# Kernel optimization log

Measured on AMD Instinct MI355X. Metric: run time of the kernel, lower is better.

The kernel has to match this reference:

```python
import jax, jax.numpy as jnp
import numpy as np

D0, D1 = 512, 512          # PSF / sensor dims (DIMS0, DIMS1)
P0, P1 = D0 // 2, D1 // 2  # pad sizes
ITERS = 20
MU1, MU2, MU3 = 1e-6, 1e-5, 1e-5
TAU = 1e-4 * 1000.0        # 0.1, as in module


def _ct(x):  # zero-pad crop-adjoint: sensor -> full size
    return jnp.pad(x, [(0, 0)] * (x.ndim - 2) + [(P0, P0), (P1, P1)])


def _c(x):  # crop full -> sensor size
    return x[..., P0:P0 + D0, P1:P1 + D1]


def _fft2(x):
    return jnp.fft.fft2(x, axes=(-2, -1))


def _ifft2(x):
    return jnp.fft.ifft2(x, axes=(-2, -1))


def _ifftshift(x):
    return jnp.fft.ifftshift(x, axes=(-2, -1))


def _fftshift(x):
    return jnp.fft.fftshift(x, axes=(-2, -1))


def _H(x, Hf):  # forward blur operator
    return jnp.real(_fftshift(_ifft2(Hf * _fft2(_ifftshift(x)))))


def _Hadj(x, Hf):  # adjoint blur operator
    return jnp.real(_fftshift(_ifft2(jnp.conj(Hf) * _fft2(_ifftshift(x)))))


def _psi(x):  # finite differences stacked on last axis -> (..., 2)
    return jnp.stack([jnp.roll(x, 1, axis=-2) - x,
                      jnp.roll(x, 1, axis=-1) - x], axis=-1)


def _psit(u):  # adjoint of _psi
    d0, d1 = u[..., 0], u[..., 1]
    return (jnp.roll(d0, -1, axis=-2) - d0) + (jnp.roll(d1, -1, axis=-1) - d1)


def _soft(v, thresh):
    return jnp.sign(v) * jnp.maximum(jnp.abs(v) - thresh, 0.0)


def _make_ltl():  # FFT of laplacian kernel (Psi^T Psi in Fourier domain)
    lapl = np.zeros((2 * D0, 2 * D1), np.float32)
    lapl[0, 0] = 4.0
    lapl[0, 1] = -1.0
    lapl[1, 0] = -1.0
    lapl[0, -1] = -1.0
    lapl[-1, 0] = -1.0
    return jnp.fft.fft2(jnp.asarray(lapl))


def setup_inputs() -> dict:
    key = jax.random.key(0)
    k1, k2 = jax.random.split(key)
    y = jax.random.uniform(k1, (8, 1, D0, D1), dtype=jnp.float32)
    h = jax.random.uniform(k2, (D0, D1), dtype=jnp.float32)
    return {"y": y, "h": h}


def reference(y, h):
    Hf = _fft2(_ifftshift(_ct(h[None])))            # (1, 2D0, 2D1) complex
    LtL = _make_ltl()                               # (2D0, 2D1) complex
    Vdiv = 1.0 / (_ct(jnp.ones((1, 1, D0, D1), y.dtype)) + MU1)
    Rdiv = 1.0 / (MU1 * jnp.abs(jnp.conj(Hf) * Hf) + MU2 * jnp.abs(LtL) + MU3)
    CTy = _ct(y)                                    # (B,1,2D0,2D1)

    B = y.shape[0]
    full = (B, 1, 2 * D0, 2 * D1)
    X = jnp.zeros(full, y.dtype)
    U = jnp.zeros(full + (2,), y.dtype)
    V = jnp.zeros(full, y.dtype)
    W = jnp.zeros(full, y.dtype)
    a1 = jnp.zeros(full, y.dtype)
    a2 = jnp.zeros(full + (2,), y.dtype)
    a3 = jnp.zeros(full, y.dtype)

    def step(carry, _):
        X, U, V, W, a1, a2, a3 = carry
        U = _soft(_psi(X) + a2 / MU2, TAU / MU2)
        V = Vdiv * (a1 + MU1 * _H(X, Hf) + CTy)
        W = jnp.maximum(a3 / MU3 + X, 0.0)
        r = (MU3 * W - a3) + _psit(MU2 * U - a2) + _Hadj(MU1 * V - a1, Hf)
        X = jnp.real(_fftshift(_ifft2(Rdiv * _fft2(_ifftshift(r)))))
        a1 = a1 + MU1 * (_H(X, Hf) - V)
        a2 = a2 + MU2 * (_psi(X) - U)
        a3 = a3 + MU3 * (X - W)
        return (X, U, V, W, a1, a2, a3), None

    (X, _, _, _, _, _, _), _ = jax.lax.scan(step, (X, U, V, W, a1, a2, a3), None, length=ITERS)
    return _c(X)
```

## Files before the change

### kernel.cpp

```cpp
#include <hip/hip_runtime.h>
#include <math.h>

#define N 1024
#define NN (1024*1024)
#define BATCH 8

static constexpr float MU1 = 1e-6f, MU2 = 1e-5f, MU3 = 1e-5f;

__device__ __forceinline__ float2 cmulf(float2 a, float2 b){
  return make_float2(a.x*b.x - a.y*b.y, a.x*b.y + a.y*b.x);
}
__device__ __forceinline__ float softf(float v, float T){
  float a = fmaxf(fabsf(v) - T, 0.f);
  return copysignf(a, v);
}
__device__ __forceinline__ int rev4_10(int p){
  return ((p&3)<<8) | (((p>>2)&3)<<6) | (((p>>4)&3)<<4) | (((p>>6)&3)<<2) | ((p>>8)&3);
}
__device__ __forceinline__ int foldc(int k){
  if (k == 0) return 0;
  if (k == 512) return 1;
  return (k < 512) ? 2*k : 2*(1024-k)+1;
}
__device__ __forceinline__ int unfoldc(int c){
  if (c < 2) return c ? 512 : 0;
  return (c & 1) ? 1024 - ((c-1)>>1) : (c>>1);
}

template<int DIR>
__device__ __forceinline__ void fft1024(float2* bufA, float2* bufB,
                                        const float2* Ws, int tid){
  float2* cur = bufA; float2* oth = bufB;
  int s = 1;
  for (int st = 0; st < 10; ++st){
    int m = 512 >> st;
    #pragma unroll
    for (int bb = 0; bb < 2; ++bb){
      int b = tid + bb*256;
      int p = b >> st;
      int q = b & (s-1);
      float2 a = cur[b];
      float2 c = cur[b + 512];
      float2 w = Ws[b & ~(s-1)];
      if (DIR > 0) w.y = -w.y;
      float2 d = make_float2(a.x - c.x, a.y - c.y);
      oth[q + s*(2*p)]   = make_float2(a.x + c.x, a.y + c.y);
      oth[q + s*(2*p+1)] = cmulf(d, w);
    }
    __syncthreads();
    float2* t = cur; cur = oth; oth = t;
    s <<= 1;
  }
}

__global__ void k_twiddle(float2* W){
  int j = blockIdx.x*blockDim.x + threadIdx.x;
  if (j < 768){
    double a = -2.0 * M_PI * (double)j / 1024.0;
    W[j] = make_float2((float)cos(a), (float)sin(a));
  }
}

__global__ void k_build_h(const float* __restrict__ h, float2* __restrict__ Z){
  int idx = blockIdx.x*256 + threadIdx.x;
  int i = idx >> 10, j = idx & 1023;
  float v = 0.f;
  if (i >= 256 && i < 768 && j >= 256 && j < 768)
    v = h[(i-256)*512 + (j-256)];
  Z[idx] = make_float2(v, 0.f);
}

__global__ void k_filters2(const float2* __restrict__ ZT, float2* __restrict__ HfC,
                           float* __restrict__ RdC){
  int id = blockIdx.x*256 + threadIdx.x;
  int p = id >> 10, cp = id & 1023;
  int ki = rev4_10(p);
  int kj = unfoldc(cp);
  float2 v = ZT[((size_t)kj << 10) | (size_t)ki];
  float sgn = ((ki + kj) & 1) ? -1.f : 1.f;
  HfC[id] = make_float2(sgn*v.x, sgn*v.y);
  double mag2 = (double)v.x*(double)v.x + (double)v.y*(double)v.y;
  double ltl = 4.0 - 2.0*cos(2.0*M_PI*(double)ki/1024.0)
                   - 2.0*cos(2.0*M_PI*(double)kj/1024.0);
  double rd = 1.0 / ((double)MU1*mag2 + (double)MU2*ltl + (double)MU3);
  RdC[id] = (float)(rd / ((double)N * (double)N));
}

__global__ void k_init(float* __restrict__ X, float* __restrict__ G0,
                       float* __restrict__ G1, float* __restrict__ K,
                       float* __restrict__ M, const float* __restrict__ y){
  int idx = blockIdx.x*256 + threadIdx.x;
  int e = idx >> 20, r = (idx >> 10) & 1023, c = idx & 1023;
  X[idx] = 0.f; G0[idx] = 0.f; G1[idx] = 0.f; K[idx] = 0.f;
  float m = 0.f;
  if (r >= 256 && r < 768 && c >= 256 && c < 768)
    m = y[(size_t)e*262144 + (size_t)(r-256)*512 + (c-256)] * (MU1/(1.f + MU1));
  M[idx] = m;
}

__global__ void k_ka(const float* __restrict__ X, float* __restrict__ G0,
                     float* __restrict__ G1){
  int idx = blockIdx.x*256 + threadIdx.x;
  int e = idx >> 20, r = (idx >> 10) & 1023, c = idx & 1023;
  size_t eb = (size_t)e * NN;
  float x   = X[idx];
  float xmr = X[eb + (size_t)((r-1)&1023)*N + c];
  float xmc = X[eb + (size_t)r*N + ((c-1)&1023)];
  float psi0 = xmr - x, psi1 = xmc - x;
  float g0 = G0[idx], g1 = G1[idx];
  const float T = 1e4f;
  float u0 = softf(2.f*psi0 - g0*(1.f/MU2), T);
  float u1 = softf(2.f*psi1 - g1*(1.f/MU2), T);
  G0[idx] = MU2*(u0 - psi0) + g0;
  G1[idx] = MU2*(u1 - psi1) + g1;
}

__global__ __launch_bounds__(256) void k_p1(const float* __restrict__ G0,
                                            const float* __restrict__ G1,
                                            const float* __restrict__ K,
                                            const float* __restrict__ M,
                                            float2* __restrict__ Z,
                                            const float2* __restrict__ Wg, int e0){
  __shared__ float2 bufA[N], bufB[N], Ws[512];
  int tid = threadIdx.x;
  int i = blockIdx.x, c = blockIdx.y, e = e0 + c;
  size_t rb  = (size_t)e*NN + (size_t)i*N;
  size_t rb1 = (size_t)e*NN + (size_t)((i+1)&1023)*N;
  size_t zb  = (size_t)c*NN + (size_t)i*N;
  for (int k = tid; k < 512; k += 256) Ws[k] = Wg[k];
  for (int j = tid; j < N; j += 256){
    int jp = (j+1) & 1023;
    float s = K[rb+j] + (G0[rb1+j] - G0[rb+j]) + (G1[rb+jp] - G1[rb+j]);
    bufA[j] = make_float2(s, M[rb+j]);
  }
  __syncthreads();
  fft1024<-1>(bufA, bufB, Ws, tid);
  for (int j = tid; j < N; j += 256) bufB[foldc(j)] = bufA[j];
  __syncthreads();
  for (int j = tid; j < N; j += 256) Z[zb+j] = bufB[j];
}

template<int DIR>
__global__ __launch_bounds__(256) void k_fft_row(float2* Z, const float2* __restrict__ Wg){
  __shared__ float2 bufA[N], bufB[N], Ws[512];
  int tid = threadIdx.x;
  size_t base = ((size_t)blockIdx.y * N + blockIdx.x) * N;
  for (int k = tid; k < 512; k += 256) Ws[k] = Wg[k];
  for (int k = tid; k < N; k += 256) bufA[k] = Z[base + k];
  __syncthreads();
  fft1024<DIR>(bufA, bufB, Ws, tid);
  for (int k = tid; k < N; k += 256) Z[base + k] = bufA[k];
}

__global__ void k_transpose_ip(float2* Z){
  __shared__ float2 ta[32][33], tb[32][33];
  int t = blockIdx.x, ti = 0;
  while (t >= 32 - ti){ t -= 32 - ti; ti++; }
  int tj = ti + t;
  size_t base = (size_t)blockIdx.y * NN;
  int ra = ti*32, ca = tj*32;
  for (int k = threadIdx.y; k < 32; k += 8){
    ta[k][threadIdx.x] = Z[base + (size_t)(ra+k)*N + ca + threadIdx.x];
    if (ti != tj)
      tb[k][threadIdx.x] = Z[base + (size_t)(ca+k)*N + ra + threadIdx.x];
  }
  __syncthreads();
  for (int k = threadIdx.y; k < 32; k += 8){
    Z[base + (size_t)(ra+k)*N + ca + threadIdx.x] = (ti!=tj) ? tb[threadIdx.x][k]
                                                             : ta[threadIdx.x][k];
    if (ti != tj)
      Z[base + (size_t)(ca+k)*N + ra + threadIdx.x] = ta[threadIdx.x][k];
  }
}

#define CPV 512
__global__ __launch_bounds__(CPV, 4) void k_colpass(float2* __restrict__ Z,
    const float2* __restrict__ HfC, const float* __restrict__ RdC,
    const float2* __restrict__ Wg){
  __shared__ float2 tile[1024][9];
  __shared__ float2 Ws[768];
  int tid = threadIdx.x;
  int blk = blockIdx.x;
  size_t zbase = (size_t)blockIdx.y*NN + ((size_t)blk<<3);
  for (int k = tid; k < 768; k += CPV) Ws[k] = Wg[k];
  for (int k = tid; k < 8192; k += CPV){
    int r = k >> 3, c = k & 7;
    tile[r][c] = Z[zbase + (size_t)r*N + c];
  }
  __syncthreads();
  #pragma unroll
  for (int s = 0; s < 5; ++s){
    int log2L = 8 - 2*s;
    int L = 1 << log2L;
    for (int k = tid; k < 2048; k += CPV){
      int c = k & 7, t = k >> 3;
      int j = t & (L-1);
      int base = ((t >> log2L) << (log2L + 2)) + j;
      float2 x0 = tile[base][c],     x1 = tile[base+L][c],
             x2 = tile[base+2*L][c], x3 = tile[base+3*L][c];
      float2 t02p = make_float2(x0.x+x2.x, x0.y+x2.y);
      float2 t02m = make_float2(x0.x-x2.x, x0.y-x2.y);
      float2 t13p = make_float2(x1.x+x3.x, x1.y+x3.y);
      float2 t13m = make_float2(x1.x-x3.x, x1.y-x3.y);
      float2 u0 = make_float2(t02p.x+t13p.x, t02p.y+t13p.y);
      float2 u2 = make_float2(t02p.x-t13p.x, t02p.y-t13p.y);
      float2 u1 = make_float2(t02m.x+t13m.y, t02m.y-t13m.x);
      float2 u3 = make_float2(t02m.x-t13m.y, t02m.y+t13m.x);
      int tw = j << (2*s);
      tile[base][c]     = u0;
      tile[base+L][c]   = cmulf(u1, Ws[tw]);
      tile[base+2*L][c] = cmulf(u2, Ws[2*tw]);
      tile[base+3*L][c] = cmulf(u3, Ws[3*tw]);
    }
    __syncthreads();
  }
  int colbase = blk << 3;
  for (int k = tid; k < 8192; k += CPV){
    int p = k >> 3, c = k & 7;
    int k1 = rev4_10(p);
    int q = rev4_10((1024 - k1) & 1023);
    int colp = colbase + c;
    int cm = (colp < 2) ? c : (c ^ 1);
    int pid = (q << 3) | cm;
    if (pid < k) continue;
    float2 Zk = tile[p][c];
    float2 Zr = tile[q][cm];
    float Sre = 0.5f*(Zk.x + Zr.x);
    float Sim = 0.5f*(Zk.y - Zr.y);
    float Mre = 0.5f*(Zk.y + Zr.y);
    float Mim = 0.5f*(Zr.x - Zk.x);
    size_t fidx = ((size_t)p << 10) | (size_t)colp;
    float2 hf = HfC[fidx];
    float rd  = RdC[fidx];
    float fr = rd*(Sre + hf.x*Mre + hf.y*Mim);
    float fi = rd*(Sim + hf.x*Mim - hf.y*Mre);
    float hr = hf.x*fr - hf.y*fi;
    float hi = hf.x*fi + hf.y*fr;
    tile[p][c] = make_float2(fr - hi, fi + hr);
    if (pid != k) tile[q][cm] = make_float2(fr + hi, hr - fi);
  }
  __syncthreads();
  #pragma unroll
  for (int s = 0; s < 5; ++s){
    int H = 1 << (2*s);
    for (int k = tid; k < 2048; k += CPV){
      int c = k & 7, t = k >> 3;
      int j = t & (H-1);
      int base = ((t >> (2*s)) << (2*s + 2)) + j;
      float2 x0 = tile[base][c],     x1 = tile[base+H][c],
             x2 = tile[base+2*H][c], x3 = tile[base+3*H][c];
      int tw = j << (8 - 2*s);
      float2 w1 = Ws[tw];   w1.y = -w1.y;
      float2 w2 = Ws[2*tw]; w2.y = -w2.y;
      float2 w3 = Ws[3*tw]; w3.y = -w3.y;
      float2 v1 = cmulf(x1, w1), v2 = cmulf(x2, w2), v3 = cmulf(x3, w3);
      float2 t02p = make_float2(x0.x+v2.x, x0.y+v2.y);
      float2 t02m = make_float2(x0.x-v2.x, x0.y-v2.y);
      float2 t13p = make_float2(v1.x+v3.x, v1.y+v3.y);
      float2 t13m = make_float2(v1.x-v3.x, v1.y-v3.y);
      tile[base][c]     = make_float2(t02p.x+t13p.x, t02p.y+t13p.y);
      tile[base+2*H][c] = make_float2(t02p.x-t13p.x, t02p.y-t13p.y);
      tile[base+H][c]   = make_float2(t02m.x-t13m.y, t02m.y+t13m.x);
      tile[base+3*H][c] = make_float2(t02m.x+t13m.y, t02m.y-t13m.x);
    }
    __syncthreads();
  }
  for (int k = tid; k < 8192; k += CPV){
    int r = k >> 3, c = k & 7;
    Z[zbase + (size_t)r*N + c] = tile[r][c];
  }
}

__global__ __launch_bounds__(256) void k_p5(const float2* __restrict__ Z,
                                            float* __restrict__ X, float* __restrict__ K,
                                            float* __restrict__ M, const float* __restrict__ y,
                                            const float2* __restrict__ Wg, int e0){
  __shared__ float2 bufA[N], bufB[N], Ws[512];
  int tid = threadIdx.x;
  int i = blockIdx.x, c = blockIdx.y, e = e0 + c;
  size_t zb = (size_t)c*NN + (size_t)i*N;
  size_t sb = (size_t)e*NN + (size_t)i*N;
  for (int k = tid; k < 512; k += 256) Ws[k] = Wg[k];
  for (int k = tid; k < N; k += 256) bufB[k] = Z[zb + k];
  __syncthreads();
  for (int k = tid; k < N; k += 256) bufA[k] = bufB[foldc(k)];
  __syncthreads();
  fft1024<1>(bufA, bufB, Ws, tid);
  bool rcent = (i >= 256 && i < 768);
  for (int j = tid; j < N; j += 256){
    float x = bufA[j].x, hx = bufA[j].y;
    X[sb+j] = x;
    float kk = K[sb+j];
    float w = fmaxf(2.f*x - kk*(1.f/MU3), 0.f);
    K[sb+j] = MU3*(w - x) + kk;
    float m = M[sb+j];
    bool cent = rcent && (j >= 256 && j < 768);
    float cty  = cent ? y[(size_t)e*262144 + (size_t)(i-256)*512 + (j-256)] : 0.f;
    float vdiv = cent ? (1.f/(1.f + MU1)) : (1.f/MU1);
    float v = vdiv*(2.f*MU1*hx - m + cty);
    M[sb+j] = MU1*(v - hx) + m;
  }
}

__global__ void k_crop(const float* __restrict__ X, float* __restrict__ out){
  int t = blockIdx.x*256 + threadIdx.x;
  int e = t >> 18;
  int r = (t >> 9) & 511;
  int c = t & 511;
  out[t] = X[(size_t)e*NN + (size_t)(r+256)*N + (c+256)];
}

extern "C" void kernel_launch(void* const* d_in, const int* in_sizes, int n_in,
                              void* d_out, int out_size, void* d_ws, size_t ws_size,
                              hipStream_t stream){
  const float* y = (const float*)d_in[0];
  const float* h = (const float*)d_in[1];
  float* out = (float*)d_out;

  size_t fplane = (size_t)BATCH * NN;
  float* X  = (float*)d_ws;
  float* G0 = X  + fplane;
  float* G1 = G0 + fplane;
  float* K  = G1 + fplane;
  float* M  = K  + fplane;
  float2* HfC  = (float2*)(M + fplane);
  float*  RdC  = (float*)(HfC + NN);
  float2* Wtab = (float2*)(RdC + NN);
  float2* Zws  = Wtab + 768;
  size_t used = (size_t)((char*)Zws - (char*)d_ws);

  int CH = 0;
  for (int c = BATCH; c >= 1; c >>= 1)
    if (used + (size_t)c * NN * sizeof(float2) <= ws_size){ CH = c; break; }
  float2* Z = (CH > 0) ? Zws : (float2*)d_out;
  if (CH == 0) CH = 1;

  k_twiddle<<<3, 256, 0, stream>>>(Wtab);
  k_build_h<<<NN/256, 256, 0, stream>>>(h, Z);
  k_fft_row<-1><<<dim3(N,1), 256, 0, stream>>>(Z, Wtab);
  k_transpose_ip<<<dim3(528,1), dim3(32,8), 0, stream>>>(Z);
  k_fft_row<-1><<<dim3(N,1), 256, 0, stream>>>(Z, Wtab);
  k_filters2<<<NN/256, 256, 0, stream>>>(Z, HfC, RdC);
  k_init<<<BATCH*NN/256, 256, 0, stream>>>(X, G0, G1, K, M, y);

  for (int t = 0; t < 20; ++t){
    k_ka<<<BATCH*NN/256, 256, 0, stream>>>(X, G0, G1);
    for (int e0 = 0; e0 < BATCH; e0 += CH){
      k_p1<<<dim3(N,CH), 256, 0, stream>>>(G0, G1, K, M, Z, Wtab, e0);
      k_colpass<<<dim3(128,CH), CPV, 0, stream>>>(Z, HfC, RdC, Wtab);
      k_p5<<<dim3(N,CH), 256, 0, stream>>>(Z, X, K, M, y, Wtab, e0);
    }
  }
  k_crop<<<(BATCH*512*512)/256, 256, 0, stream>>>(X, out);
}
```

Measured before the change: 3.848 ms.

## Fuse dual-update into FFT passes, register radix-16 column FFT, blocked filter layout

Removes the standalone k_ka pass. The G0 (row-difference) dual update moves into the first row-FFT kernel, which recomputes the neighbour row's update and uses ping-pong G0 buffers to avoid read/write races. The G1 update moves into the inverse row pass, and the final crop is folded into the last iteration. The column FFT kernel is restructured into register-held radix-16 stages with fewer barriers, an XOR-swizzled shared tile, and filter arrays reordered to match the block layout. The cost is extra redundant loads for the neighbour-row G0 and X values, plus one more full-plane buffer.

New measurement: 3.769 ms. -2.0%, faster.

```diff
diff --git a/kernel.cpp b/kernel.cpp
--- a/kernel.cpp
+++ b/kernel.cpp
@@ -10,6 +10,7 @@
 __device__ __forceinline__ float2 cmulf(float2 a, float2 b){
   return make_float2(a.x*b.x - a.y*b.y, a.x*b.y + a.y*b.x);
 }
+__device__ __forceinline__ float2 conjf(float2 a){ return make_float2(a.x, -a.y); }
 __device__ __forceinline__ float softf(float v, float T){
   float a = fmaxf(fabsf(v) - T, 0.f);
   return copysignf(a, v);
@@ -26,6 +27,25 @@
   if (c < 2) return c ? 512 : 0;
   return (c & 1) ? 1024 - ((c-1)>>1) : (c>>1);
 }
+
+#define BF4F(x0,x1,x2,x3,u0,u1,u2,u3) { \
+  float2 t02p = make_float2((x0).x+(x2).x, (x0).y+(x2).y); \
+  float2 t02m = make_float2((x0).x-(x2).x, (x0).y-(x2).y); \
+  float2 t13p = make_float2((x1).x+(x3).x, (x1).y+(x3).y); \
+  float2 t13m = make_float2((x1).x-(x3).x, (x1).y-(x3).y); \
+  u0 = make_float2(t02p.x+t13p.x, t02p.y+t13p.y); \
+  u2 = make_float2(t02p.x-t13p.x, t02p.y-t13p.y); \
+  u1 = make_float2(t02m.x+t13m.y, t02m.y-t13m.x); \
+  u3 = make_float2(t02m.x-t13m.y, t02m.y+t13m.x); }
+#define BF4I(x0,x1,x2,x3,u0,u1,u2,u3) { \
+  float2 t02p = make_float2((x0).x+(x2).x, (x0).y+(x2).y); \
+  float2 t02m = make_float2((x0).x-(x2).x, (x0).y-(x2).y); \
+  float2 t13p = make_float2((x1).x+(x3).x, (x1).y+(x3).y); \
+  float2 t13m = make_float2((x1).x-(x3).x, (x1).y-(x3).y); \
+  u0 = make_float2(t02p.x+t13p.x, t02p.y+t13p.y); \
+  u2 = make_float2(t02p.x-t13p.x, t02p.y-t13p.y); \
+  u1 = make_float2(t02m.x-t13m.y, t02m.y+t13m.x); \
+  u3 = make_float2(t02m.x+t13m.y, t02m.y-t13m.x); }
 
 template<int DIR>
 __device__ __forceinline__ void fft1024(float2* bufA, float2* bufB,
@@ -70,52 +90,41 @@
   Z[idx] = make_float2(v, 0.f);
 }
 
-__global__ void k_filters2(const float2* __restrict__ ZT, float2* __restrict__ HfC,
-                           float* __restrict__ RdC){
+__global__ void k_filters2(const float2* __restrict__ ZT, float2* __restrict__ HfCb,
+                           float* __restrict__ RdCb){
   int id = blockIdx.x*256 + threadIdx.x;
-  int p = id >> 10, cp = id & 1023;
+  int blk = id >> 13;
+  int rem = id & 8191;
+  int p = rem >> 3, c = rem & 7;
+  int colp = (blk << 3) | c;
   int ki = rev4_10(p);
-  int kj = unfoldc(cp);
+  int kj = unfoldc(colp);
   float2 v = ZT[((size_t)kj << 10) | (size_t)ki];
   float sgn = ((ki + kj) & 1) ? -1.f : 1.f;
-  HfC[id] = make_float2(sgn*v.x, sgn*v.y);
+  HfCb[id] = make_float2(sgn*v.x, sgn*v.y);
   double mag2 = (double)v.x*(double)v.x + (double)v.y*(double)v.y;
   double ltl = 4.0 - 2.0*cos(2.0*M_PI*(double)ki/1024.0)
                    - 2.0*cos(2.0*M_PI*(double)kj/1024.0);
   double rd = 1.0 / ((double)MU1*mag2 + (double)MU2*ltl + (double)MU3);
-  RdC[id] = (float)(rd / ((double)N * (double)N));
-}
-
-__global__ void k_init(float* __restrict__ X, float* __restrict__ G0,
-                       float* __restrict__ G1, float* __restrict__ K,
-                       float* __restrict__ M, const float* __restrict__ y){
+  RdCb[id] = (float)(rd / ((double)N * (double)N));
+}
+
+__global__ void k_init(float* __restrict__ X, float* __restrict__ G1,
+                       float* __restrict__ K, float* __restrict__ M,
+                       float* __restrict__ G0a, float* __restrict__ G0b,
+                       const float* __restrict__ y){
   int idx = blockIdx.x*256 + threadIdx.x;
   int e = idx >> 20, r = (idx >> 10) & 1023, c = idx & 1023;
-  X[idx] = 0.f; G0[idx] = 0.f; G1[idx] = 0.f; K[idx] = 0.f;
+  X[idx] = 0.f; G1[idx] = 0.f; K[idx] = 0.f; G0a[idx] = 0.f; G0b[idx] = 0.f;
   float m = 0.f;
   if (r >= 256 && r < 768 && c >= 256 && c < 768)
     m = y[(size_t)e*262144 + (size_t)(r-256)*512 + (c-256)] * (MU1/(1.f + MU1));
   M[idx] = m;
 }
 
-__global__ void k_ka(const float* __restrict__ X, float* __restrict__ G0,
-                     float* __restrict__ G1){
-  int idx = blockIdx.x*256 + threadIdx.x;
-  int e = idx >> 20, r = (idx >> 10) & 1023, c = idx & 1023;
-  size_t eb = (size_t)e * NN;
-  float x   = X[idx];
-  float xmr = X[eb + (size_t)((r-1)&1023)*N + c];
-  float xmc = X[eb + (size_t)r*N + ((c-1)&1023)];
-  float psi0 = xmr - x, psi1 = xmc - x;
-  float g0 = G0[idx], g1 = G1[idx];
-  const float T = 1e4f;
-  float u0 = softf(2.f*psi0 - g0*(1.f/MU2), T);
-  float u1 = softf(2.f*psi1 - g1*(1.f/MU2), T);
-  G0[idx] = MU2*(u0 - psi0) + g0;
-  G1[idx] = MU2*(u1 - psi1) + g1;
-}
-
-__global__ __launch_bounds__(256) void k_p1(const float* __restrict__ G0,
+__global__ __launch_bounds__(256) void k_pA(const float* __restrict__ X,
+                                            const float* __restrict__ G0r,
+                                            float* __restrict__ G0w,
                                             const float* __restrict__ G1,
                                             const float* __restrict__ K,
                                             const float* __restrict__ M,
@@ -123,14 +132,28 @@
                                             const float2* __restrict__ Wg, int e0){
   __shared__ float2 bufA[N], bufB[N], Ws[512];
   int tid = threadIdx.x;
-  int i = blockIdx.x, c = blockIdx.y, e = e0 + c;
-  size_t rb  = (size_t)e*NN + (size_t)i*N;
-  size_t rb1 = (size_t)e*NN + (size_t)((i+1)&1023)*N;
-  size_t zb  = (size_t)c*NN + (size_t)i*N;
+  int bid = blockIdx.x;
+  int i = ((bid & 7) << 7) + (bid >> 3);
+  int ce = blockIdx.y, e = e0 + ce;
+  size_t eb  = (size_t)e*NN;
+  size_t rb  = eb + (size_t)i*N;
+  size_t rbm = eb + (size_t)((i-1)&1023)*N;
+  size_t rbp = eb + (size_t)((i+1)&1023)*N;
+  size_t zb  = (size_t)ce*NN + (size_t)i*N;
   for (int k = tid; k < 512; k += 256) Ws[k] = Wg[k];
+  const float T = 1e4f;
   for (int j = tid; j < N; j += 256){
+    float xm = X[rbm+j], x = X[rb+j], xp = X[rbp+j];
+    float psi0  = xm - x;
+    float psi0p = x - xp;
+    float g0  = G0r[rb+j], g0p = G0r[rbp+j];
+    float u0  = softf(2.f*psi0  - g0 *(1.f/MU2), T);
+    float u0p = softf(2.f*psi0p - g0p*(1.f/MU2), T);
+    float g0n  = MU2*(u0  - psi0 ) + g0;
+    float g0np = MU2*(u0p - psi0p) + g0p;
+    G0w[rb+j] = g0n;
     int jp = (j+1) & 1023;
-    float s = K[rb+j] + (G0[rb1+j] - G0[rb+j]) + (G1[rb+jp] - G1[rb+j]);
+    float s = K[rb+j] + (g0np - g0n) + (G1[rb+jp] - G1[rb+j]);
     bufA[j] = make_float2(s, M[rb+j]);
   }
   __syncthreads();
@@ -173,11 +196,12 @@
   }
 }
 
+#define TADDR(r,c) ((((r)*9) + (c)) ^ (((r) & 16) >> 1))
 #define CPV 512
 __global__ __launch_bounds__(CPV, 4) void k_colpass(float2* __restrict__ Z,
-    const float2* __restrict__ HfC, const float* __restrict__ RdC,
+    const float2* __restrict__ HfCb, const float* __restrict__ RdCb,
     const float2* __restrict__ Wg){
-  __shared__ float2 tile[1024][9];
+  __shared__ float2 tile[9216];
   __shared__ float2 Ws[768];
   int tid = threadIdx.x;
   int blk = blockIdx.x;
@@ -185,100 +209,205 @@
   for (int k = tid; k < 768; k += CPV) Ws[k] = Wg[k];
   for (int k = tid; k < 8192; k += CPV){
     int r = k >> 3, c = k & 7;
-    tile[r][c] = Z[zbase + (size_t)r*N + c];
-  }
-  __syncthreads();
-  #pragma unroll
-  for (int s = 0; s < 5; ++s){
-    int log2L = 8 - 2*s;
-    int L = 1 << log2L;
-    for (int k = tid; k < 2048; k += CPV){
-      int c = k & 7, t = k >> 3;
-      int j = t & (L-1);
-      int base = ((t >> log2L) << (log2L + 2)) + j;
-      float2 x0 = tile[base][c],     x1 = tile[base+L][c],
-             x2 = tile[base+2*L][c], x3 = tile[base+3*L][c];
-      float2 t02p = make_float2(x0.x+x2.x, x0.y+x2.y);
-      float2 t02m = make_float2(x0.x-x2.x, x0.y-x2.y);
-      float2 t13p = make_float2(x1.x+x3.x, x1.y+x3.y);
-      float2 t13m = make_float2(x1.x-x3.x, x1.y-x3.y);
-      float2 u0 = make_float2(t02p.x+t13p.x, t02p.y+t13p.y);
-      float2 u2 = make_float2(t02p.x-t13p.x, t02p.y-t13p.y);
-      float2 u1 = make_float2(t02m.x+t13m.y, t02m.y-t13m.x);
-      float2 u3 = make_float2(t02m.x-t13m.y, t02m.y+t13m.x);
-      int tw = j << (2*s);
-      tile[base][c]     = u0;
-      tile[base+L][c]   = cmulf(u1, Ws[tw]);
-      tile[base+2*L][c] = cmulf(u2, Ws[2*tw]);
-      tile[base+3*L][c] = cmulf(u3, Ws[3*tw]);
-    }
-    __syncthreads();
-  }
-  int colbase = blk << 3;
-  for (int k = tid; k < 8192; k += CPV){
-    int p = k >> 3, c = k & 7;
-    int k1 = rev4_10(p);
-    int q = rev4_10((1024 - k1) & 1023);
-    int colp = colbase + c;
-    int cm = (colp < 2) ? c : (c ^ 1);
-    int pid = (q << 3) | cm;
-    if (pid < k) continue;
-    float2 Zk = tile[p][c];
-    float2 Zr = tile[q][cm];
-    float Sre = 0.5f*(Zk.x + Zr.x);
-    float Sim = 0.5f*(Zk.y - Zr.y);
-    float Mre = 0.5f*(Zk.y + Zr.y);
-    float Mim = 0.5f*(Zr.x - Zk.x);
-    size_t fidx = ((size_t)p << 10) | (size_t)colp;
-    float2 hf = HfC[fidx];
-    float rd  = RdC[fidx];
-    float fr = rd*(Sre + hf.x*Mre + hf.y*Mim);
-    float fi = rd*(Sim + hf.x*Mim - hf.y*Mre);
-    float hr = hf.x*fr - hf.y*fi;
-    float hi = hf.x*fi + hf.y*fr;
-    tile[p][c] = make_float2(fr - hi, fi + hr);
-    if (pid != k) tile[q][cm] = make_float2(fr + hi, hr - fi);
-  }
-  __syncthreads();
-  #pragma unroll
-  for (int s = 0; s < 5; ++s){
-    int H = 1 << (2*s);
-    for (int k = tid; k < 2048; k += CPV){
-      int c = k & 7, t = k >> 3;
-      int j = t & (H-1);
-      int base = ((t >> (2*s)) << (2*s + 2)) + j;
-      float2 x0 = tile[base][c],     x1 = tile[base+H][c],
-             x2 = tile[base+2*H][c], x3 = tile[base+3*H][c];
-      int tw = j << (8 - 2*s);
-      float2 w1 = Ws[tw];   w1.y = -w1.y;
-      float2 w2 = Ws[2*tw]; w2.y = -w2.y;
-      float2 w3 = Ws[3*tw]; w3.y = -w3.y;
-      float2 v1 = cmulf(x1, w1), v2 = cmulf(x2, w2), v3 = cmulf(x3, w3);
-      float2 t02p = make_float2(x0.x+v2.x, x0.y+v2.y);
-      float2 t02m = make_float2(x0.x-v2.x, x0.y-v2.y);
-      float2 t13p = make_float2(v1.x+v3.x, v1.y+v3.y);
-      float2 t13m = make_float2(v1.x-v3.x, v1.y-v3.y);
-      tile[base][c]     = make_float2(t02p.x+t13p.x, t02p.y+t13p.y);
-      tile[base+2*H][c] = make_float2(t02p.x-t13p.x, t02p.y-t13p.y);
-      tile[base+H][c]   = make_float2(t02m.x-t13m.y, t02m.y+t13m.x);
-      tile[base+3*H][c] = make_float2(t02m.x+t13m.y, t02m.y-t13m.x);
-    }
-    __syncthreads();
-  }
+    tile[TADDR(r,c)] = Z[zbase + (size_t)r*N + c];
+  }
+  __syncthreads();
+  {
+    int c = tid & 7, j2 = tid >> 3;
+    float2 v[4][4];
+    #pragma unroll
+    for (int a = 0; a < 4; ++a)
+      #pragma unroll
+      for (int b = 0; b < 4; ++b)
+        v[a][b] = tile[TADDR(j2 + 64*b + 256*a, c)];
+    #pragma unroll
+    for (int b = 0; b < 4; ++b){
+      int j1 = j2 + 64*b;
+      float2 u0,u1,u2,u3;
+      BF4F(v[0][b],v[1][b],v[2][b],v[3][b],u0,u1,u2,u3);
+      v[0][b] = u0;
+      v[1][b] = cmulf(u1, Ws[j1]);
+      v[2][b] = cmulf(u2, Ws[2*j1]);
+      v[3][b] = cmulf(u3, Ws[3*j1]);
+    }
+    int tw = j2 << 2;
+    #pragma unroll
+    for (int a = 0; a < 4; ++a){
+      float2 u0,u1,u2,u3;
+      BF4F(v[a][0],v[a][1],v[a][2],v[a][3],u0,u1,u2,u3);
+      tile[TADDR(j2 + 256*a, c)]       = u0;
+      tile[TADDR(j2 + 64 + 256*a, c)]  = cmulf(u1, Ws[tw]);
+      tile[TADDR(j2 + 128 + 256*a, c)] = cmulf(u2, Ws[2*tw]);
+      tile[TADDR(j2 + 192 + 256*a, c)] = cmulf(u3, Ws[3*tw]);
+    }
+  }
+  __syncthreads();
+  {
+    int c = tid & 7, vv = tid >> 3;
+    int B2 = vv >> 2, j2 = vv & 3;
+    int r0 = 64*B2 + j2;
+    float2 v[4][4];
+    #pragma unroll
+    for (int a = 0; a < 4; ++a)
+      #pragma unroll
+      for (int b = 0; b < 4; ++b)
+        v[a][b] = tile[TADDR(r0 + 4*b + 16*a, c)];
+    #pragma unroll
+    for (int b = 0; b < 4; ++b){
+      int tw = (j2 + 4*b) << 4;
+      float2 u0,u1,u2,u3;
+      BF4F(v[0][b],v[1][b],v[2][b],v[3][b],u0,u1,u2,u3);
+      v[0][b] = u0;
+      v[1][b] = cmulf(u1, Ws[tw]);
+      v[2][b] = cmulf(u2, Ws[2*tw]);
+      v[3][b] = cmulf(u3, Ws[3*tw]);
+    }
+    int tw3 = j2 << 6;
+    #pragma unroll
+    for (int a = 0; a < 4; ++a){
+      float2 u0,u1,u2,u3;
+      BF4F(v[a][0],v[a][1],v[a][2],v[a][3],u0,u1,u2,u3);
+      tile[TADDR(r0 + 16*a, c)]      = u0;
+      tile[TADDR(r0 + 16*a + 4, c)]  = cmulf(u1, Ws[tw3]);
+      tile[TADDR(r0 + 16*a + 8, c)]  = cmulf(u2, Ws[2*tw3]);
+      tile[TADDR(r0 + 16*a + 12, c)] = cmulf(u3, Ws[3*tw3]);
+    }
+  }
+  __syncthreads();
+  for (int k = tid; k < 2048; k += CPV){
+    int c = k & 7, t = k >> 3;
+    int r = 4*t;
+    float2 x0 = tile[TADDR(r,c)],   x1 = tile[TADDR(r+1,c)];
+    float2 x2 = tile[TADDR(r+2,c)], x3 = tile[TADDR(r+3,c)];
+    float2 u0,u1,u2,u3;
+    BF4F(x0,x1,x2,x3,u0,u1,u2,u3);
+    tile[TADDR(r,c)] = u0; tile[TADDR(r+1,c)] = u1;
+    tile[TADDR(r+2,c)] = u2; tile[TADDR(r+3,c)] = u3;
+  }
+  __syncthreads();
+  {
+    size_t fbase = (size_t)blk << 13;
+    for (int k = tid; k < 8192; k += CPV){
+      int p = k >> 3, c = k & 7;
+      int k1 = rev4_10(p);
+      int q = rev4_10((1024 - k1) & 1023);
+      int colp = (blk << 3) + c;
+      int cm = (colp < 2) ? c : (c ^ 1);
+      int pid = (q << 3) | cm;
+      if (pid < k) continue;
+      float2 Zk = tile[TADDR(p,c)];
+      float2 Zr = tile[TADDR(q,cm)];
+      float Sre = 0.5f*(Zk.x + Zr.x);
+      float Sim = 0.5f*(Zk.y - Zr.y);
+      float Mre = 0.5f*(Zk.y + Zr.y);
+      float Mim = 0.5f*(Zr.x - Zk.x);
+      float2 hf = HfCb[fbase + k];
+      float rd  = RdCb[fbase + k];
+      float fr = rd*(Sre + hf.x*Mre + hf.y*Mim);
+      float fi = rd*(Sim + hf.x*Mim - hf.y*Mre);
+      float hr = hf.x*fr - hf.y*fi;
+      float hi = hf.x*fi + hf.y*fr;
+      tile[TADDR(p,c)] = make_float2(fr - hi, fi + hr);
+      if (pid != k) tile[TADDR(q,cm)] = make_float2(fr + hi, hr - fi);
+    }
+  }
+  __syncthreads();
+  {
+    int c = tid & 7, G = tid >> 3;
+    int r0 = 16*G;
+    float2 v[4][4];
+    #pragma unroll
+    for (int a = 0; a < 4; ++a)
+      #pragma unroll
+      for (int b = 0; b < 4; ++b)
+        v[a][b] = tile[TADDR(r0 + 4*a + b, c)];
+    #pragma unroll
+    for (int a = 0; a < 4; ++a){
+      float2 u0,u1,u2,u3;
+      BF4I(v[a][0],v[a][1],v[a][2],v[a][3],u0,u1,u2,u3);
+      v[a][0]=u0; v[a][1]=u1; v[a][2]=u2; v[a][3]=u3;
+    }
+    #pragma unroll
+    for (int b = 0; b < 4; ++b){
+      int tw = b << 6;
+      float2 x0 = v[0][b];
+      float2 x1 = cmulf(v[1][b], conjf(Ws[tw]));
+      float2 x2 = cmulf(v[2][b], conjf(Ws[2*tw]));
+      float2 x3 = cmulf(v[3][b], conjf(Ws[3*tw]));
+      float2 u0,u1,u2,u3;
+      BF4I(x0,x1,x2,x3,u0,u1,u2,u3);
+      tile[TADDR(r0 + b, c)]      = u0;
+      tile[TADDR(r0 + 4 + b, c)]  = u1;
+      tile[TADDR(r0 + 8 + b, c)]  = u2;
+      tile[TADDR(r0 + 12 + b, c)] = u3;
+    }
+  }
+  __syncthreads();
+  {
+    int c = tid & 7, vv = tid >> 3;
+    int T3 = vv >> 4, jj = vv & 15;
+    int r0 = 256*T3 + jj;
+    float2 v[4][4];
+    #pragma unroll
+    for (int a = 0; a < 4; ++a)
+      #pragma unroll
+      for (int b = 0; b < 4; ++b)
+        v[a][b] = tile[TADDR(r0 + 16*a + 64*b, c)];
+    int tw2 = jj << 4;
+    #pragma unroll
+    for (int b = 0; b < 4; ++b){
+      float2 x0 = v[0][b];
+      float2 x1 = cmulf(v[1][b], conjf(Ws[tw2]));
+      float2 x2 = cmulf(v[2][b], conjf(Ws[2*tw2]));
+      float2 x3 = cmulf(v[3][b], conjf(Ws[3*tw2]));
+      float2 u0,u1,u2,u3;
+      BF4I(x0,x1,x2,x3,u0,u1,u2,u3);
+      v[0][b]=u0; v[1][b]=u1; v[2][b]=u2; v[3][b]=u3;
+    }
+    #pragma unroll
+    for (int a = 0; a < 4; ++a){
+      int tw = (jj + 16*a) << 2;
+      float2 x0 = v[a][0];
+      float2 x1 = cmulf(v[a][1], conjf(Ws[tw]));
+      float2 x2 = cmulf(v[a][2], conjf(Ws[2*tw]));
+      float2 x3 = cmulf(v[a][3], conjf(Ws[3*tw]));
+      float2 u0,u1,u2,u3;
+      BF4I(x0,x1,x2,x3,u0,u1,u2,u3);
+      tile[TADDR(r0 + 16*a, c)]       = u0;
+      tile[TADDR(r0 + 16*a + 64, c)]  = u1;
+      tile[TADDR(r0 + 16*a + 128, c)] = u2;
+      tile[TADDR(r0 + 16*a + 192, c)] = u3;
+    }
+  }
+  __syncthreads();
+  for (int k = tid; k < 2048; k += CPV){
+    int c = k & 7, t = k >> 3;
+    float2 x0 = tile[TADDR(t,c)];
+    float2 x1 = cmulf(tile[TADDR(t+256,c)], conjf(Ws[t]));
+    float2 x2 = cmulf(tile[TADDR(t+512,c)], conjf(Ws[2*t]));
+    float2 x3 = cmulf(tile[TADDR(t+768,c)], conjf(Ws[3*t]));
+    float2 u0,u1,u2,u3;
+    BF4I(x0,x1,x2,x3,u0,u1,u2,u3);
+    tile[TADDR(t,c)] = u0;     tile[TADDR(t+256,c)] = u1;
+    tile[TADDR(t+512,c)] = u2; tile[TADDR(t+768,c)] = u3;
+  }
+  __syncthreads();
   for (int k = tid; k < 8192; k += CPV){
     int r = k >> 3, c = k & 7;
-    Z[zbase + (size_t)r*N + c] = tile[r][c];
+    Z[zbase + (size_t)r*N + c] = tile[TADDR(r,c)];
   }
 }
 
 __global__ __launch_bounds__(256) void k_p5(const float2* __restrict__ Z,
                                             float* __restrict__ X, float* __restrict__ K,
-                                            float* __restrict__ M, const float* __restrict__ y,
+                                            float* __restrict__ M, float* __restrict__ G1,
+                                            const float* __restrict__ y,
+                                            float* __restrict__ out, int writeOut,
                                             const float2* __restrict__ Wg, int e0){
   __shared__ float2 bufA[N], bufB[N], Ws[512];
   int tid = threadIdx.x;
-  int i = blockIdx.x, c = blockIdx.y, e = e0 + c;
-  size_t zb = (size_t)c*NN + (size_t)i*N;
+  int i = blockIdx.x, ce = blockIdx.y, e = e0 + ce;
+  size_t zb = (size_t)ce*NN + (size_t)i*N;
   size_t sb = (size_t)e*NN + (size_t)i*N;
   for (int k = tid; k < 512; k += 256) Ws[k] = Wg[k];
   for (int k = tid; k < N; k += 256) bufB[k] = Z[zb + k];
@@ -287,6 +416,7 @@
   __syncthreads();
   fft1024<1>(bufA, bufB, Ws, tid);
   bool rcent = (i >= 256 && i < 768);
+  const float T = 1e4f;
   for (int j = tid; j < N; j += 256){
     float x = bufA[j].x, hx = bufA[j].y;
     X[sb+j] = x;
@@ -299,6 +429,13 @@
     float vdiv = cent ? (1.f/(1.f + MU1)) : (1.f/MU1);
     float v = vdiv*(2.f*MU1*hx - m + cty);
     M[sb+j] = MU1*(v - hx) + m;
+    float xm = bufA[(j-1)&1023].x;
+    float psi1 = xm - x;
+    float g1 = G1[sb+j];
+    float u1 = softf(2.f*psi1 - g1*(1.f/MU2), T);
+    G1[sb+j] = MU2*(u1 - psi1) + g1;
+    if (writeOut && cent)
+      out[(size_t)e*262144 + (size_t)(i-256)*512 + (j-256)] = x;
   }
 }
 
@@ -318,21 +455,23 @@
   float* out = (float*)d_out;
 
   size_t fplane = (size_t)BATCH * NN;
-  float* X  = (float*)d_ws;
-  float* G0 = X  + fplane;
-  float* G1 = G0 + fplane;
-  float* K  = G1 + fplane;
-  float* M  = K  + fplane;
-  float2* HfC  = (float2*)(M + fplane);
-  float*  RdC  = (float*)(HfC + NN);
-  float2* Wtab = (float2*)(RdC + NN);
+  float* X   = (float*)d_ws;
+  float* G1  = X   + fplane;
+  float* K   = G1  + fplane;
+  float* M   = K   + fplane;
+  float* G0a = M   + fplane;
+  float* G0b = G0a + fplane;
+  float2* HfCb = (float2*)(G0b + fplane);
+  float*  RdCb = (float*)(HfCb + NN);
+  float2* Wtab = (float2*)(RdCb + NN);
   float2* Zws  = Wtab + 768;
   size_t used = (size_t)((char*)Zws - (char*)d_ws);
 
   int CH = 0;
   for (int c = BATCH; c >= 1; c >>= 1)
     if (used + (size_t)c * NN * sizeof(float2) <= ws_size){ CH = c; break; }
-  float2* Z = (CH > 0) ? Zws : (float2*)d_out;
+  bool fallback = (CH == 0);
+  float2* Z = fallback ? (float2*)d_out : Zws;
   if (CH == 0) CH = 1;
 
   k_twiddle<<<3, 256, 0, stream>>>(Wtab);
@@ -340,16 +479,19 @@
   k_fft_row<-1><<<dim3(N,1), 256, 0, stream>>>(Z, Wtab);
   k_transpose_ip<<<dim3(528,1), dim3(32,8), 0, stream>>>(Z);
   k_fft_row<-1><<<dim3(N,1), 256, 0, stream>>>(Z, Wtab);
-  k_filters2<<<NN/256, 256, 0, stream>>>(Z, HfC, RdC);
-  k_init<<<BATCH*NN/256, 256, 0, stream>>>(X, G0, G1, K, M, y);
+  k_filters2<<<NN/256, 256, 0, stream>>>(Z, HfCb, RdCb);
+  k_init<<<BATCH*NN/256, 256, 0, stream>>>(X, G1, K, M, G0a, G0b, y);
 
   for (int t = 0; t < 20; ++t){
-    k_ka<<<BATCH*NN/256, 256, 0, stream>>>(X, G0, G1);
+    const float* G0r = (t & 1) ? G0b : G0a;
+    float*       G0w = (t & 1) ? G0a : G0b;
+    int wo = (t == 19 && !fallback) ? 1 : 0;
     for (int e0 = 0; e0 < BATCH; e0 += CH){
-      k_p1<<<dim3(N,CH), 256, 0, stream>>>(G0, G1, K, M, Z, Wtab, e0);
-      k_colpass<<<dim3(128,CH), CPV, 0, stream>>>(Z, HfC, RdC, Wtab);
-      k_p5<<<dim3(N,CH), 256, 0, stream>>>(Z, X, K, M, y, Wtab, e0);
-    }
-  }
-  k_crop<<<(BATCH*512*512)/256, 256, 0, stream>>>(X, out);
-}
+      k_pA<<<dim3(N,CH), 256, 0, stream>>>(X, G0r, G0w, G1, K, M, Z, Wtab, e0);
+      k_colpass<<<dim3(128,CH), CPV, 0, stream>>>(Z, HfCb, RdCb, Wtab);
+      k_p5<<<dim3(N,CH), 256, 0, stream>>>(Z, X, K, M, G1, y, out, wo, Wtab, e0);
+    }
+  }
+  if (fallback)
+    k_crop<<<(BATCH*512*512)/256, 256, 0, stream>>>(X, out);
+}
```
